# Performance work log

Measured on AMD Instinct MI355X. Metric: run time of the kernel, lower is better.

Reference implementation:

```python
import jax, jax.numpy as jnp
import numpy as np

NEG_SLOPE = 0.2


def gat_layer(x_src, x_dst, src, dst, W, a_src, a_dst, b, n_dst, H, C):
    # Linear transform: [Ns, H, C] / [Nd, H, C]
    h_s = (x_src @ W).reshape(-1, H, C)
    h_d = (x_dst @ W).reshape(-1, H, C)
    # Per-edge attention logits: a . [x_i || x_j] (x_i = dst/target, x_j = src)
    e = jnp.einsum('ehc,hc->eh', h_s[src], a_src) + jnp.einsum('ehc,hc->eh', h_d[dst], a_dst)
    e = jax.nn.leaky_relu(e, NEG_SLOPE)  # [E, H]
    # Segment softmax over destination neighborhoods
    m = jax.ops.segment_max(e, dst, num_segments=n_dst)          # [Nd, H]
    ex = jnp.exp(e - m[dst])
    denom = jax.ops.segment_sum(ex, dst, num_segments=n_dst)    # [Nd, H]
    alpha = ex / denom[dst]                                      # [E, H]
    # Weighted scatter-sum aggregation
    out = jax.ops.segment_sum(alpha[:, :, None] * h_s[src], dst, num_segments=n_dst)
    return out.reshape(n_dst, H * C) + b


def setup_inputs() -> dict:
    key = jax.random.key(0)
    ks = jax.random.split(key, 16)
    N, F_IN, OUT = 200000, 602, 41
    N1, N1D, E1 = 120000, 30000, 960000
    N2D, E2 = 6000, 192000
    s = 0.05
    return {
        'x': jax.random.normal(ks[0], (N, F_IN), jnp.float32),
        'n_id1': jax.random.randint(ks[1], (N1,), 0, N),
        'res_n_id1': jax.random.randint(ks[2], (N1D,), 0, N1),
        'edge_src1': jax.random.randint(ks[3], (E1,), 0, N1),
        'edge_dst1': jax.random.randint(ks[4], (E1,), 0, N1D),
        'res_n_id2': jax.random.randint(ks[5], (N2D,), 0, N1D),
        'edge_src2': jax.random.randint(ks[6], (E2,), 0, N1D),
        'edge_dst2': jax.random.randint(ks[7], (E2,), 0, N2D),
        'W1': jax.random.normal(ks[8], (F_IN, 64), jnp.float32) * s,
        'att_src1': jax.random.normal(ks[9], (8, 8), jnp.float32) * s,
        'att_dst1': jax.random.normal(ks[10], (8, 8), jnp.float32) * s,
        'bias1': jax.random.normal(ks[11], (64,), jnp.float32) * s,
        'W2': jax.random.normal(ks[12], (64, OUT), jnp.float32) * s,
        'att_src2': jax.random.normal(ks[13], (1, OUT), jnp.float32) * s,
        'att_dst2': jax.random.normal(ks[14], (1, OUT), jnp.float32) * s,
        'bias2': jax.random.normal(ks[15], (OUT,), jnp.float32) * s,
    }


def reference(x, n_id1, res_n_id1, edge_src1, edge_dst1, res_n_id2, edge_src2,
              edge_dst2, W1, att_src1, att_dst1, bias1, W2, att_src2, att_dst2, bias2):
    # Block 1: gather frontier, GATConv(in -> 8, heads=8, concat) -> [N1D, 64]
    h = x[n_id1]
    h = gat_layer(h, h[res_n_id1], edge_src1, edge_dst1,
                  W1, att_src1, att_dst1, bias1, res_n_id1.shape[0], 8, 8)
    h = jax.nn.elu(h)
    # (dropout p=0.6 is identity in eval mode)
    # Block 2: GATConv(64 -> out, heads=1) -> [N2D, out]
    h = gat_layer(h, h[res_n_id2], edge_src2, edge_dst2,
                  W2, att_src2, att_dst2, bias2, res_n_id2.shape[0], 1, W2.shape[1])
    return jax.nn.log_softmax(h, axis=1)
```

## Files before the change

kernel.cpp:

```cpp
#include <hip/hip_runtime.h>
#include <hip/hip_bf16.h>
#include <math.h>

typedef __attribute__((ext_vector_type(8))) short short8;
typedef __attribute__((ext_vector_type(4))) float float4v;

__device__ __forceinline__ float wave_max64(float v) {
#pragma unroll
  for (int o = 32; o > 0; o >>= 1) v = fmaxf(v, __shfl_xor(v, o));
  return v;
}
__device__ __forceinline__ float wave_sum64(float v) {
#pragma unroll
  for (int o = 32; o > 0; o >>= 1) v += __shfl_xor(v, o);
  return v;
}
__device__ __forceinline__ float lrelu02(float v) { return v > 0.f ? v : 0.2f * v; }
__device__ __forceinline__ short bf16_rne(float f) {
  unsigned u = __builtin_bit_cast(unsigned, f);
  unsigned r = (u + 0x7FFFu + ((u >> 16) & 1u)) >> 16;
  return (short)r;
}

__global__ void hist_prepack_kernel(const int* __restrict__ dst1, const int* __restrict__ dst2,
                                    int* __restrict__ counts, const float* __restrict__ W,
                                    short* __restrict__ Wp, int E1, int E2, int N1D, int nbE) {
  int b = blockIdx.x;
  if (b < nbE) {
    int e = b * 256 + threadIdx.x;
    if (e < E1) atomicAdd(&counts[dst1[e]], 1);
    else if (e < E1 + E2) atomicAdd(&counts[N1D + dst2[e - E1]], 1);
  } else {
    int idx = (b - nbE) * 256 + threadIdx.x;
    if (idx >= 19 * 4 * 64) return;
    int lane = idx & 63;
    int t = (idx >> 6) & 3;
    int s = idx >> 8;
    int quad = lane >> 4, n = t * 16 + (lane & 15);
    short8 v;
#pragma unroll
    for (int j = 0; j < 8; j++) {
      int k = s * 32 + quad * 8 + j;
      v[j] = (k < 602) ? bf16_rne(W[k * 64 + n]) : (short)0;
    }
    *((short8*)Wp + idx) = v;
  }
}

__global__ __launch_bounds__(256) void scan1_kernel(const int* __restrict__ counts,
                                                    int* __restrict__ offs,
                                                    int* __restrict__ bsum, int n) {
  __shared__ int ws[4], wpre[4];
  int tid = threadIdx.x, lane = tid & 63, w = tid >> 6;
  int i = blockIdx.x * 256 + tid;
  int v = (i < n) ? counts[i] : 0;
  int x = v;
#pragma unroll
  for (int o = 1; o < 64; o <<= 1) {
    int y = __shfl_up(x, o);
    if (lane >= o) x += y;
  }
  if (lane == 63) ws[w] = x;
  __syncthreads();
  if (tid == 0) {
    int run = 0;
#pragma unroll
    for (int k = 0; k < 4; k++) { wpre[k] = run; run += ws[k]; }
    bsum[blockIdx.x] = run;
  }
  __syncthreads();
  if (i < n) offs[i] = x - v + wpre[w];
}

__global__ __launch_bounds__(256) void scan2_kernel(int* __restrict__ bsum, int nb) {
  __shared__ int ws[4], wpre[4];
  int tid = threadIdx.x, lane = tid & 63, w = tid >> 6;
  int v = (tid < nb) ? bsum[tid] : 0;
  int x = v;
#pragma unroll
  for (int o = 1; o < 64; o <<= 1) {
    int y = __shfl_up(x, o);
    if (lane >= o) x += y;
  }
  if (lane == 63) ws[w] = x;
  __syncthreads();
  if (tid == 0) {
    int run = 0;
#pragma unroll
    for (int k = 0; k < 4; k++) { wpre[k] = run; run += ws[k]; }
  }
  __syncthreads();
  if (tid < nb) bsum[tid] = x - v + wpre[w];
}

__global__ __launch_bounds__(256) void scan3_kernel(int* __restrict__ offs,
                                                    const int* __restrict__ bsum,
                                                    int n, int etot) {
  int i = blockIdx.x * 256 + threadIdx.x;
  if (i < n) offs[i] += bsum[blockIdx.x];
  if (i == 0) offs[n] = etot;
}

__global__ void scatter_kernel(const int* __restrict__ dst1, const int* __restrict__ src1,
                               const int* __restrict__ dst2, const int* __restrict__ src2,
                               const int* __restrict__ offs, int* __restrict__ cursor,
                               int* __restrict__ epay, int E1, int E2, int N1D) {
  int e = blockIdx.x * blockDim.x + threadIdx.x;
  if (e < E1) {
    int d = dst1[e];
    int pos = offs[d] + atomicAdd(&cursor[d], 1);
    epay[pos] = src1[e];
  } else if (e < E1 + E2) {
    int e2 = e - E1;
    int d = N1D + dst2[e2];
    int pos = offs[d] + atomicAdd(&cursor[d], 1);
    epay[pos] = src2[e2];
  }
}

__global__ __launch_bounds__(256) void gemm1_mfma_kernel(const float* __restrict__ x,
                                                         const int* __restrict__ n_id,
                                                         const short* __restrict__ Wp,
                                                         float* __restrict__ out, int M) {
  constexpr int K = 602, NSTEP = 19;
  int tid = threadIdx.x;
  int wid = tid >> 6, lane = tid & 63;
  int quad = lane >> 4, mrow = lane & 15;
  int r = blockIdx.x * 64 + wid * 16 + mrow;
  int grow = n_id[r < M ? r : M - 1];
  const float* xrow = x + (size_t)grow * K;
  float4v acc[4] = {{0.f, 0.f, 0.f, 0.f}, {0.f, 0.f, 0.f, 0.f},
                    {0.f, 0.f, 0.f, 0.f}, {0.f, 0.f, 0.f, 0.f}};
  for (int s = 0; s < NSTEP; s++) {
    int k0 = s * 32 + quad * 8;
    float af[8];
    if (k0 + 8 <= K) {
#pragma unroll
      for (int j = 0; j < 8; j += 2) {
        float2 v = *(const float2*)(xrow + k0 + j);
        af[j] = v.x;
        af[j + 1] = v.y;
      }
    } else {
#pragma unroll
      for (int j = 0; j < 8; j++) af[j] = (k0 + j < K) ? xrow[k0 + j] : 0.f;
    }
    short8 a;
#pragma unroll
    for (int j = 0; j < 8; j++) a[j] = bf16_rne(af[j]);
    const short8* wp = (const short8*)Wp + (size_t)s * 256 + lane;
#pragma unroll
    for (int t = 0; t < 4; t++) {
      short8 b = wp[t * 64];
      acc[t] = __builtin_amdgcn_mfma_f32_16x16x32_bf16(a, b, acc[t], 0, 0, 0);
    }
  }
  int rb = blockIdx.x * 64 + wid * 16;
#pragma unroll
  for (int t = 0; t < 4; t++) {
#pragma unroll
    for (int j = 0; j < 4; j++) {
      int rr = rb + quad * 4 + j;
      if (rr < M) out[(size_t)rr * 64 + t * 16 + mrow] = acc[t][j];
    }
  }
}

__global__ void attn_src1_kernel(const float* __restrict__ hs1, const float* __restrict__ a,
                                 float* __restrict__ s, int N) {
  int t = blockIdx.x * blockDim.x + threadIdx.x;
  if (t >= N * 8) return;
  int i = t >> 3, h = t & 7;
  const float* p = hs1 + (size_t)i * 64 + h * 8;
  const float* q = a + h * 8;
  float acc = 0.f;
#pragma unroll
  for (int j = 0; j < 8; j++) acc += p[j] * q[j];
  s[t] = acc;
}

__global__ __launch_bounds__(256) void agg1_kernel(
    const int* __restrict__ offs, const int* __restrict__ srcs,
    const float* __restrict__ s_src, const int* __restrict__ res,
    const float* __restrict__ ad, const float* __restrict__ hs1,
    const float* __restrict__ bias, float* __restrict__ h1, int n_dst) {
  int wid = (blockIdx.x * blockDim.x + threadIdx.x) >> 6;
  if (wid >= n_dst) return;
  int lane = threadIdx.x & 63;
  int h = lane >> 3;
  int node = res[wid];
  float v = hs1[(size_t)node * 64 + lane] * ad[lane];
  v += __shfl_xor(v, 1);
  v += __shfl_xor(v, 2);
  v += __shfl_xor(v, 4);
  float sd = v;
  int beg = offs[wid], end = offs[wid + 1];
  float mx = -1e30f, den = 0.f, acc = 0.f;
  for (int i = beg; i < end; i += 8) {
    int m = end - i; if (m > 8) m = 8;
    int sr[8]; float ss[8], row[8];
#pragma unroll
    for (int j = 0; j < 8; j++) sr[j] = srcs[i + (j < m ? j : 0)];
#pragma unroll
    for (int j = 0; j < 8; j++) ss[j] = s_src[sr[j] * 8 + h];
#pragma unroll
    for (int j = 0; j < 8; j++) row[j] = hs1[(size_t)sr[j] * 64 + lane];
    float p[8];
#pragma unroll
    for (int j = 0; j < 8; j++) p[j] = (j < m) ? lrelu02(ss[j] + sd) : -1e30f;
    float bm = mx;
#pragma unroll
    for (int j = 0; j < 8; j++) bm = fmaxf(bm, p[j]);
    float scale = __expf(mx - bm);
    den *= scale;
    acc *= scale;
#pragma unroll
    for (int j = 0; j < 8; j++) {
      float w = __expf(p[j] - bm);
      den += w;
      acc += w * row[j];
    }
    mx = bm;
  }
  float val = (end > beg) ? acc / den : 0.f;
  val += bias[lane];
  val = val > 0.f ? val : __expf(val) - 1.f;
  h1[(size_t)wid * 64 + lane] = val;
}

__global__ __launch_bounds__(256) void gemm2_kernel(const float* __restrict__ h1,
                                                    const float* __restrict__ W2,
                                                    const float* __restrict__ a_src,
                                                    float* __restrict__ hs2,
                                                    float* __restrict__ ssrc, int M) {
  constexpr int C = 41;
  __shared__ float Ws[64 * C];
  for (int i = threadIdx.x; i < 64 * C; i += 256) Ws[i] = W2[i];
  __syncthreads();
  int lane = threadIdx.x & 63;
  int r = blockIdx.x * 4 + (threadIdx.x >> 6);
  if (r >= M) return;
  const float* row = h1 + (size_t)r * 64;
  float acc = 0.f;
  if (lane < C) {
#pragma unroll 8
    for (int k = 0; k < 64; k++) acc += row[k] * Ws[k * C + lane];
  }
  float t = (lane < C) ? acc * a_src[lane] : 0.f;
  t = wave_sum64(t);
  if (lane == 0) ssrc[r] = t;
  if (lane < C) hs2[(size_t)r * C + lane] = acc;
}

__global__ __launch_bounds__(256) void agg2_kernel(
    const int* __restrict__ offs, const int* __restrict__ srcs,
    const float* __restrict__ s_src, const int* __restrict__ res,
    const float* __restrict__ ad, const float* __restrict__ hs2,
    const float* __restrict__ bias, float* __restrict__ out, int n_dst) {
  constexpr int C = 41;
  int wid = (blockIdx.x * blockDim.x + threadIdx.x) >> 6;
  if (wid >= n_dst) return;
  int lane = threadIdx.x & 63;
  bool act = lane < C;
  int node = res[wid];
  float dv = act ? hs2[(size_t)node * C + lane] * ad[lane] : 0.f;
  float sd = wave_sum64(dv);
  int beg = offs[wid], end = offs[wid + 1];
  float mx = -1e30f, den = 0.f, acc = 0.f;
  for (int i = beg; i < end; i += 8) {
    int m = end - i; if (m > 8) m = 8;
    int sr[8]; float ss[8], row[8];
#pragma unroll
    for (int j = 0; j < 8; j++) sr[j] = srcs[i + (j < m ? j : 0)];
#pragma unroll
    for (int j = 0; j < 8; j++) ss[j] = s_src[sr[j]];
#pragma unroll
    for (int j = 0; j < 8; j++) row[j] = act ? hs2[(size_t)sr[j] * C + lane] : 0.f;
    float p[8];
#pragma unroll
    for (int j = 0; j < 8; j++) p[j] = (j < m) ? lrelu02(ss[j] + sd) : -1e30f;
    float bm = mx;
#pragma unroll
    for (int j = 0; j < 8; j++) bm = fmaxf(bm, p[j]);
    float scale = __expf(mx - bm);
    den *= scale;
    acc *= scale;
#pragma unroll
    for (int j = 0; j < 8; j++) {
      float w = __expf(p[j] - bm);
      den += w;
      acc += w * row[j];
    }
    mx = bm;
  }
  float val = (end > beg) ? acc / den : 0.f;
  if (act) val += bias[lane];
  float lv = act ? val : -1e30f;
  float m2 = wave_max64(lv);
  float ex = act ? __expf(val - m2) : 0.f;
  float ssum = wave_sum64(ex);
  if (act) out[(size_t)wid * C + lane] = val - m2 - __logf(ssum);
}

extern "C" void kernel_launch(void* const* d_in, const int* in_sizes, int n_in,
                              void* d_out, int out_size, void* d_ws, size_t ws_size,
                              hipStream_t stream) {
  const float* x    = (const float*)d_in[0];
  const int* n_id1  = (const int*)d_in[1];
  const int* res1   = (const int*)d_in[2];
  const int* esrc1  = (const int*)d_in[3];
  const int* edst1  = (const int*)d_in[4];
  const int* res2   = (const int*)d_in[5];
  const int* esrc2  = (const int*)d_in[6];
  const int* edst2  = (const int*)d_in[7];
  const float* W1   = (const float*)d_in[8];
  const float* as1  = (const float*)d_in[9];
  const float* ad1  = (const float*)d_in[10];
  const float* b1   = (const float*)d_in[11];
  const float* W2   = (const float*)d_in[12];
  const float* as2  = (const float*)d_in[13];
  const float* ad2  = (const float*)d_in[14];
  const float* b2   = (const float*)d_in[15];
  float* out = (float*)d_out;

  const int N1  = in_sizes[1];
  const int N1D = in_sizes[2];
  const int E1  = in_sizes[3];
  const int N2D = in_sizes[5];
  const int E2  = in_sizes[6];
  const int NTOT = N1D + N2D;
  const int ETOT = E1 + E2;

  char* w = (char*)d_ws;
  size_t off = 0;
  auto alloc = [&](size_t bytes) -> void* {
    void* p = (void*)(w + off);
    off += (bytes + 255) & ~(size_t)255;
    return p;
  };
  float* hs1   = (float*)alloc((size_t)N1 * 64 * 4);
  float* ssrc1 = (float*)alloc((size_t)N1 * 8 * 4);
  float* h1    = (float*)alloc((size_t)N1D * 64 * 4);
  float* hs2   = (float*)alloc((size_t)N1D * 41 * 4);
  float* ssrc2 = (float*)alloc((size_t)N1D * 4);
  int* counts  = (int*)alloc((size_t)2 * NTOT * 4);
  int* cursor  = counts + NTOT;
  int* offs    = (int*)alloc((size_t)(NTOT + 1) * 4);
  int* bsum    = (int*)alloc((size_t)256 * 4);
  int* epay    = (int*)alloc((size_t)ETOT * 4);
  short* Wp    = (short*)alloc((size_t)19 * 4 * 64 * 8 * 2);
  (void)ws_size; (void)n_in; (void)out_size;

  hipMemsetAsync(counts, 0, (size_t)2 * NTOT * 4, stream);

  const int nbE = (ETOT + 255) / 256;
  const int nb = (NTOT + 255) / 256;
  hist_prepack_kernel<<<nbE + 19, 256, 0, stream>>>(edst1, edst2, counts, W1, Wp, E1, E2, N1D, nbE);
  scan1_kernel<<<nb, 256, 0, stream>>>(counts, offs, bsum, NTOT);
  scan2_kernel<<<1, 256, 0, stream>>>(bsum, nb);
  scan3_kernel<<<nb, 256, 0, stream>>>(offs, bsum, NTOT, ETOT);
  scatter_kernel<<<nbE, 256, 0, stream>>>(edst1, esrc1, edst2, esrc2, offs, cursor, epay, E1, E2, N1D);

  gemm1_mfma_kernel<<<(N1 + 63) / 64, 256, 0, stream>>>(x, n_id1, Wp, hs1, N1);
  attn_src1_kernel<<<(N1 * 8 + 255) / 256, 256, 0, stream>>>(hs1, as1, ssrc1, N1);
  agg1_kernel<<<(N1D + 3) / 4, 256, 0, stream>>>(offs, epay, ssrc1, res1, ad1, hs1, b1, h1, N1D);

  gemm2_kernel<<<(N1D + 3) / 4, 256, 0, stream>>>(h1, W2, as2, hs2, ssrc2, N1D);
  agg2_kernel<<<(N2D + 3) / 4, 256, 0, stream>>>(offs + N1D, epay, ssrc2, res2, ad2, hs2, b2, out, N2D);
}
```

Before: 840.4 us.

## Fuse attention-src dot into GEMM1, GEMM2 into agg1, drop cursor array

Computes the per-head source attention scores in the GEMM1 epilogue with lane shuffles, which removes the attn_src1 kernel and its reread of hs1. Folds the second linear layer and its attention dot into the end of agg1 by broadcasting the 64-wide row with shuffles against W2 held in shared memory, so the h1 intermediate is never written and gemm2 is removed. The scatter now bumps the offsets array itself with atomics, so entry k ends at the end of segment k and consumers read [offs[k-1], offs[k]). This removes the cursor array, part of the memset and one offset read. In exchange agg1 loads W2 into shared memory in every block and runs 64 shuffle-FMA steps per destination node.

```diff
diff --git a/kernel.cpp b/kernel.cpp
--- a/kernel.cpp
+++ b/kernel.cpp
@@ -94,26 +94,22 @@
 }
 
 __global__ __launch_bounds__(256) void scan3_kernel(int* __restrict__ offs,
-                                                    const int* __restrict__ bsum,
-                                                    int n, int etot) {
+                                                    const int* __restrict__ bsum, int n) {
   int i = blockIdx.x * 256 + threadIdx.x;
   if (i < n) offs[i] += bsum[blockIdx.x];
-  if (i == 0) offs[n] = etot;
 }
 
 __global__ void scatter_kernel(const int* __restrict__ dst1, const int* __restrict__ src1,
                                const int* __restrict__ dst2, const int* __restrict__ src2,
-                               const int* __restrict__ offs, int* __restrict__ cursor,
-                               int* __restrict__ epay, int E1, int E2, int N1D) {
+                               int* __restrict__ offs, int* __restrict__ epay,
+                               int E1, int E2, int N1D) {
   int e = blockIdx.x * blockDim.x + threadIdx.x;
   if (e < E1) {
-    int d = dst1[e];
-    int pos = offs[d] + atomicAdd(&cursor[d], 1);
+    int pos = atomicAdd(&offs[dst1[e]], 1);
     epay[pos] = src1[e];
   } else if (e < E1 + E2) {
     int e2 = e - E1;
-    int d = N1D + dst2[e2];
-    int pos = offs[d] + atomicAdd(&cursor[d], 1);
+    int pos = atomicAdd(&offs[N1D + dst2[e2]], 1);
     epay[pos] = src2[e2];
   }
 }
@@ -121,7 +117,9 @@
 __global__ __launch_bounds__(256) void gemm1_mfma_kernel(const float* __restrict__ x,
                                                          const int* __restrict__ n_id,
                                                          const short* __restrict__ Wp,
-                                                         float* __restrict__ out, int M) {
+                                                         const float* __restrict__ as1,
+                                                         float* __restrict__ out,
+                                                         float* __restrict__ ssrc, int M) {
   constexpr int K = 602, NSTEP = 19;
   int tid = threadIdx.x;
   int wid = tid >> 6, lane = tid & 63;
@@ -164,26 +162,37 @@
       if (rr < M) out[(size_t)rr * 64 + t * 16 + mrow] = acc[t][j];
     }
   }
-}
-
-__global__ void attn_src1_kernel(const float* __restrict__ hs1, const float* __restrict__ a,
-                                 float* __restrict__ s, int N) {
-  int t = blockIdx.x * blockDim.x + threadIdx.x;
-  if (t >= N * 8) return;
-  int i = t >> 3, h = t & 7;
-  const float* p = hs1 + (size_t)i * 64 + h * 8;
-  const float* q = a + h * 8;
-  float acc = 0.f;
-#pragma unroll
-  for (int j = 0; j < 8; j++) acc += p[j] * q[j];
-  s[t] = acc;
+  int hi = mrow >> 3, u = mrow & 7;
+  float a_s[4];
+#pragma unroll
+  for (int t = 0; t < 4; t++) a_s[t] = as1[(2 * t + hi) * 8 + u];
+#pragma unroll
+  for (int t = 0; t < 4; t++) {
+#pragma unroll
+    for (int j = 0; j < 4; j++) {
+      float p = acc[t][j] * a_s[t];
+      p += __shfl_xor(p, 1);
+      p += __shfl_xor(p, 2);
+      p += __shfl_xor(p, 4);
+      if (u == j) {
+        int rr = rb + quad * 4 + j;
+        if (rr < M) ssrc[(size_t)rr * 8 + 2 * t + hi] = p;
+      }
+    }
+  }
 }
 
 __global__ __launch_bounds__(256) void agg1_kernel(
     const int* __restrict__ offs, const int* __restrict__ srcs,
     const float* __restrict__ s_src, const int* __restrict__ res,
     const float* __restrict__ ad, const float* __restrict__ hs1,
-    const float* __restrict__ bias, float* __restrict__ h1, int n_dst) {
+    const float* __restrict__ bias, const float* __restrict__ W2,
+    const float* __restrict__ as2, float* __restrict__ hs2,
+    float* __restrict__ ssrc2, int n_dst) {
+  constexpr int C = 41;
+  __shared__ float Ws[64 * C];
+  for (int i = threadIdx.x; i < 64 * C; i += 256) Ws[i] = W2[i];
+  __syncthreads();
   int wid = (blockIdx.x * blockDim.x + threadIdx.x) >> 6;
   if (wid >= n_dst) return;
   int lane = threadIdx.x & 63;
@@ -194,7 +203,8 @@
   v += __shfl_xor(v, 2);
   v += __shfl_xor(v, 4);
   float sd = v;
-  int beg = offs[wid], end = offs[wid + 1];
+  int beg = wid ? offs[wid - 1] : 0;
+  int end = offs[wid];
   float mx = -1e30f, den = 0.f, acc = 0.f;
   for (int i = beg; i < end; i += 8) {
     int m = end - i; if (m > 8) m = 8;
@@ -225,31 +235,18 @@
   float val = (end > beg) ? acc / den : 0.f;
   val += bias[lane];
   val = val > 0.f ? val : __expf(val) - 1.f;
-  h1[(size_t)wid * 64 + lane] = val;
-}
-
-__global__ __launch_bounds__(256) void gemm2_kernel(const float* __restrict__ h1,
-                                                    const float* __restrict__ W2,
-                                                    const float* __restrict__ a_src,
-                                                    float* __restrict__ hs2,
-                                                    float* __restrict__ ssrc, int M) {
-  constexpr int C = 41;
-  __shared__ float Ws[64 * C];
-  for (int i = threadIdx.x; i < 64 * C; i += 256) Ws[i] = W2[i];
-  __syncthreads();
-  int lane = threadIdx.x & 63;
-  int r = blockIdx.x * 4 + (threadIdx.x >> 6);
-  if (r >= M) return;
-  const float* row = h1 + (size_t)r * 64;
-  float acc = 0.f;
-  if (lane < C) {
-#pragma unroll 8
-    for (int k = 0; k < 64; k++) acc += row[k] * Ws[k * C + lane];
-  }
-  float t = (lane < C) ? acc * a_src[lane] : 0.f;
-  t = wave_sum64(t);
-  if (lane == 0) ssrc[r] = t;
-  if (lane < C) hs2[(size_t)r * C + lane] = acc;
+  bool act = lane < C;
+  int cl = act ? lane : C - 1;
+  float acc2 = 0.f;
+#pragma unroll
+  for (int k = 0; k < 64; k++) {
+    float hk = __shfl(val, k);
+    acc2 += hk * Ws[k * C + cl];
+  }
+  float t2 = act ? acc2 * as2[lane] : 0.f;
+  float s2 = wave_sum64(t2);
+  if (lane == 0) ssrc2[wid] = s2;
+  if (act) hs2[(size_t)wid * C + lane] = acc2;
 }
 
 __global__ __launch_bounds__(256) void agg2_kernel(
@@ -265,7 +262,8 @@
   int node = res[wid];
   float dv = act ? hs2[(size_t)node * C + lane] * ad[lane] : 0.f;
   float sd = wave_sum64(dv);
-  int beg = offs[wid], end = offs[wid + 1];
+  int beg = offs[wid - 1];
+  int end = offs[wid];
   float mx = -1e30f, den = 0.f, acc = 0.f;
   for (int i = beg; i < end; i += 8) {
     int m = end - i; if (m > 8) m = 8;
@@ -340,31 +338,28 @@
   };
   float* hs1   = (float*)alloc((size_t)N1 * 64 * 4);
   float* ssrc1 = (float*)alloc((size_t)N1 * 8 * 4);
-  float* h1    = (float*)alloc((size_t)N1D * 64 * 4);
   float* hs2   = (float*)alloc((size_t)N1D * 41 * 4);
   float* ssrc2 = (float*)alloc((size_t)N1D * 4);
-  int* counts  = (int*)alloc((size_t)2 * NTOT * 4);
-  int* cursor  = counts + NTOT;
-  int* offs    = (int*)alloc((size_t)(NTOT + 1) * 4);
+  int* counts  = (int*)alloc((size_t)NTOT * 4);
+  int* offs    = (int*)alloc((size_t)NTOT * 4);
   int* bsum    = (int*)alloc((size_t)256 * 4);
   int* epay    = (int*)alloc((size_t)ETOT * 4);
   short* Wp    = (short*)alloc((size_t)19 * 4 * 64 * 8 * 2);
   (void)ws_size; (void)n_in; (void)out_size;
 
-  hipMemsetAsync(counts, 0, (size_t)2 * NTOT * 4, stream);
+  hipMemsetAsync(counts, 0, (size_t)NTOT * 4, stream);
 
   const int nbE = (ETOT + 255) / 256;
   const int nb = (NTOT + 255) / 256;
   hist_prepack_kernel<<<nbE + 19, 256, 0, stream>>>(edst1, edst2, counts, W1, Wp, E1, E2, N1D, nbE);
   scan1_kernel<<<nb, 256, 0, stream>>>(counts, offs, bsum, NTOT);
   scan2_kernel<<<1, 256, 0, stream>>>(bsum, nb);
-  scan3_kernel<<<nb, 256, 0, stream>>>(offs, bsum, NTOT, ETOT);
-  scatter_kernel<<<nbE, 256, 0, stream>>>(edst1, esrc1, edst2, esrc2, offs, cursor, epay, E1, E2, N1D);
-
-  gemm1_mfma_kernel<<<(N1 + 63) / 64, 256, 0, stream>>>(x, n_id1, Wp, hs1, N1);
-  attn_src1_kernel<<<(N1 * 8 + 255) / 256, 256, 0, stream>>>(hs1, as1, ssrc1, N1);
-  agg1_kernel<<<(N1D + 3) / 4, 256, 0, stream>>>(offs, epay, ssrc1, res1, ad1, hs1, b1, h1, N1D);
-
-  gemm2_kernel<<<(N1D + 3) / 4, 256, 0, stream>>>(h1, W2, as2, hs2, ssrc2, N1D);
+  scan3_kernel<<<nb, 256, 0, stream>>>(offs, bsum, NTOT);
+  scatter_kernel<<<nbE, 256, 0, stream>>>(edst1, esrc1, edst2, esrc2, offs, epay, E1, E2, N1D);
+
+  gemm1_mfma_kernel<<<(N1 + 63) / 64, 256, 0, stream>>>(x, n_id1, Wp, as1, hs1, ssrc1, N1);
+  agg1_kernel<<<(N1D + 3) / 4, 256, 0, stream>>>(offs, epay, ssrc1, res1, ad1, hs1, b1,
+                                                 W2, as2, hs2, ssrc2, N1D);
+
   agg2_kernel<<<(N2D + 3) / 4, 256, 0, stream>>>(offs + N1D, epay, ssrc2, res2, ad2, hs2, b2, out, N2D);
 }
```

Result: no change. 856.9 us (+2.0%).
